# Performance work log

Hardware: AMD Instinct MI355X
Metric: run time of the kernel (lower is better)

The kernel has to match this reference:

```python
import jax, jax.numpy as jnp
import numpy as np

N = 50000
E = 800000
D = 512
H = 256
K = 16
COLLAPSE_REG = 1.0


def setup_inputs() -> dict:
    key = jax.random.key(0)
    ks = jax.random.split(key, 8)
    embeddings = jax.random.normal(ks[0], (N, D), dtype=jnp.float32)
    edge_src = jax.random.randint(ks[1], (E,), 0, N, dtype=jnp.int32)
    edge_dst = jax.random.randint(ks[2], (E,), 0, N, dtype=jnp.int32)
    # GCNConv params (glorot-ish scaling)
    W1 = jax.random.normal(ks[3], (D, H), dtype=jnp.float32) / np.sqrt(D)
    b1 = jnp.zeros((H,), dtype=jnp.float32)
    W2 = jax.random.normal(ks[4], (H, H), dtype=jnp.float32) / np.sqrt(H)
    b2 = jnp.zeros((H,), dtype=jnp.float32)
    Wa = jax.random.normal(ks[5], (H, K), dtype=jnp.float32) / np.sqrt(H)
    ba = jnp.zeros((K,), dtype=jnp.float32)
    return {"embeddings": embeddings, "edge_src": edge_src, "edge_dst": edge_dst,
            "W1": W1, "b1": b1, "W2": W2, "b2": b2, "Wa": Wa, "ba": ba}


def _gcn_conv(x, W, b, src, dst, dis):
    # PyG GCNConv: transform then D^{-1/2}(A+I)D^{-1/2} aggregation + bias.
    x = x @ W                                   # [N, out]
    norm = dis[src] * dis[dst]                  # [E]
    agg = jax.ops.segment_sum(x[src] * norm[:, None], dst, num_segments=N)
    agg = agg + (dis * dis)[:, None] * x        # self-loop term
    return agg + b


def reference(embeddings, edge_src, edge_dst, W1, b1, W2, b2, Wa, ba):
    # symmetric-norm degrees with self-loops (edge weight 1)
    deg = 1.0 + jax.ops.segment_sum(jnp.ones((E,), jnp.float32), edge_dst, num_segments=N)
    dis = jax.lax.rsqrt(deg)                    # deg > 0 always (self-loop)

    x = jax.nn.selu(_gcn_conv(embeddings, W1, b1, edge_src, edge_dst, dis))
    x_skip = x  # dropout is identity in eval
    x = jax.nn.selu(_gcn_conv(x, W2, b2, edge_src, edge_dst, dis))
    x = x + x_skip
    assignments = jax.nn.softmax(x @ Wa + ba, axis=1)   # [N, K]

    # ---- DMoN losses (faithful to original, incl. scalar normalizer) ----
    degrees = jax.ops.segment_sum(jnp.ones((E,), jnp.float32), edge_src, num_segments=N)  # row sums of A
    m = degrees.sum() / 2.0
    AS = jax.ops.segment_sum(assignments[edge_dst], edge_src, num_segments=N)  # A @ S, [N, K]
    trace_pooled = jnp.sum(assignments * AS)    # trace(S^T A S)
    dS = degrees @ assignments                  # [K]
    normalizer = jnp.dot(dS, dS) / (2.0 * m)    # scalar (as in original code)
    spectral_loss = -(trace_pooled - K * normalizer) / (2.0 * m)

    cluster_sizes = assignments.sum(axis=0)     # [K]
    collapse_loss = jnp.linalg.norm(cluster_sizes) / N * jnp.sqrt(jnp.float32(K)) - 1.0
    entropy = -jnp.sum(assignments * jnp.log(assignments + 1e-8)) / N
    entropy_loss = -0.1 * entropy
    total_loss = spectral_loss + COLLAPSE_REG * collapse_loss + entropy_loss

    pooled = (assignments / (cluster_sizes + 1e-8)).T @ embeddings  # [K, D]
    return (assignments, pooled, spectral_loss, COLLAPSE_REG * collapse_loss, total_loss, entropy_loss)
```

## Files before the change

kernel.cpp:

```cpp
#include <hip/hip_runtime.h>
#include <hip/hip_fp16.h>
#include <math.h>

#define NN 50000
#define EE 800000
#define DD 512
#define HH 256
#define KK 16
#define NB_SCAN 196

typedef _Float16 half8_t __attribute__((ext_vector_type(8)));
typedef float f32x4 __attribute__((ext_vector_type(4)));

__global__ void zero_kernel(int* __restrict__ p, int n) {
    int i = blockIdx.x * blockDim.x + threadIdx.x;
    if (i < n) p[i] = 0;
}

__global__ void count_kernel(const int4* __restrict__ src4, const int4* __restrict__ dst4,
                             int* __restrict__ indeg, int* __restrict__ outdeg) {
    int e = blockIdx.x * blockDim.x + threadIdx.x;
    if (e < EE / 4) {
        int4 s = src4[e], d = dst4[e];
        atomicAdd(&outdeg[s.x], 1); atomicAdd(&outdeg[s.y], 1);
        atomicAdd(&outdeg[s.z], 1); atomicAdd(&outdeg[s.w], 1);
        atomicAdd(&indeg[d.x], 1);  atomicAdd(&indeg[d.y], 1);
        atomicAdd(&indeg[d.z], 1);  atomicAdd(&indeg[d.w], 1);
    }
}

__global__ void scan_p1(const int* __restrict__ in, int* __restrict__ part, int n,
                        const int* __restrict__ outdeg, float* __restrict__ dis,
                        float* __restrict__ degf) {
    __shared__ int tile[256];
    int t = threadIdx.x;
    int i = blockIdx.x * 256 + t;
    int v = (i < n) ? in[i] : 0;
    tile[t] = v;
    if (i < n) {
        dis[i]  = 1.0f / sqrtf(1.0f + (float)v);
        degf[i] = (float)outdeg[i];
    }
    __syncthreads();
    for (int o = 128; o > 0; o >>= 1) {
        if (t < o) tile[t] += tile[t + o];
        __syncthreads();
    }
    if (t == 0) part[blockIdx.x] = tile[0];
}

__global__ void scan_p2(int* __restrict__ part, int nb, int* __restrict__ off_end) {
    __shared__ int tile[256];
    int t = threadIdx.x;
    int v = (t < nb) ? part[t] : 0;
    tile[t] = v;
    __syncthreads();
    for (int o = 1; o < 256; o <<= 1) {
        int x = (t >= o) ? tile[t - o] : 0;
        __syncthreads();
        tile[t] += x;
        __syncthreads();
    }
    if (t < nb) part[t] = tile[t] - v;
    if (t == 255) *off_end = tile[255];
}

__global__ void scan_p3(const int* __restrict__ in, const int* __restrict__ part,
                        int* __restrict__ out, int n) {
    __shared__ int tile[256];
    int t = threadIdx.x;
    int i = blockIdx.x * 256 + t;
    int v = (i < n) ? in[i] : 0;
    tile[t] = v;
    __syncthreads();
    for (int o = 1; o < 256; o <<= 1) {
        int x = (t >= o) ? tile[t - o] : 0;
        __syncthreads();
        tile[t] += x;
        __syncthreads();
    }
    if (i < n) out[i] = part[blockIdx.x] + tile[t] - v;
}

__global__ void scatter_kernel(const int4* __restrict__ src4, const int4* __restrict__ dst4,
                               const int* __restrict__ off, int* __restrict__ cur,
                               int* __restrict__ nbr) {
    int e = blockIdx.x * blockDim.x + threadIdx.x;
    if (e < EE / 4) {
        int4 s = src4[e], d = dst4[e];
        int p;
        p = atomicAdd(&cur[d.x], 1); nbr[off[d.x] + p] = s.x;
        p = atomicAdd(&cur[d.y], 1); nbr[off[d.y] + p] = s.y;
        p = atomicAdd(&cur[d.z], 1); nbr[off[d.z] + p] = s.z;
        p = atomicAdd(&cur[d.w], 1); nbr[off[d.w] + p] = s.w;
    }
}

__global__ void transpose_w(const float* __restrict__ W1, __half* __restrict__ Wt1,
                            const float* __restrict__ W2, __half* __restrict__ Wt2) {
    int i = blockIdx.x * 256 + threadIdx.x;
    if (i < DD * HH) {
        int k = i / HH, n = i % HH;
        Wt1[(size_t)n * DD + k] = __float2half(W1[i]);
    } else {
        int j = i - DD * HH;
        int k = j / HH, n = j % HH;
        Wt2[(size_t)n * HH + k] = __float2half(W2[j]);
    }
}

template <typename TA, int KDIM>
__global__ __launch_bounds__(256) void mfma_gemm(const TA* __restrict__ A,
                                                 const __half* __restrict__ Bt,
                                                 __half* __restrict__ C, int M) {
    constexpr bool F32 = sizeof(TA) == 4;
    constexpr int SROW = F32 ? 36 : 40;
    constexpr int EPG  = F32 ? 4 : 8;
    constexpr int GPR  = 32 / EPG;
    constexpr int RPP  = 256 / GPR;
    constexpr int NP   = 128 / RPP;
    constexpr int KI   = KDIM / 32;

    __shared__ TA As[2][128 * SROW];

    int t = threadIdx.x;
    int wave = t >> 6, lane = t & 63, quad = lane >> 4, l16 = lane & 15;
    int row0 = blockIdx.x * 128, col0 = blockIdx.y * 128;
    int wm = (wave & 1) * 64, wn = (wave >> 1) * 64;
    int srow = t / GPR, sg = t % GPR;

    f32x4 acc[4][4] = {};
    uint4 sreg[NP];
    uint4 bcur[4];

    const __half* brow[4];
#pragma unroll
    for (int ni = 0; ni < 4; ni++)
        brow[ni] = Bt + (size_t)(col0 + wn + ni * 16 + l16) * KDIM + quad * 8;

    auto gloadA = [&](int k0) {
#pragma unroll
        for (int p = 0; p < NP; p++) {
            int gr = row0 + p * RPP + srow;
            if (gr < M)
                sreg[p] = *(const uint4*)(A + (size_t)gr * KDIM + k0 + sg * EPG);
            else
                sreg[p] = make_uint4(0, 0, 0, 0);
        }
    };
    auto sstore = [&](int buf) {
#pragma unroll
        for (int p = 0; p < NP; p++)
            *(uint4*)&As[buf][(p * RPP + srow) * SROW + sg * EPG] = sreg[p];
    };

    gloadA(0);
#pragma unroll
    for (int ni = 0; ni < 4; ni++) bcur[ni] = *(const uint4*)(brow[ni]);
    sstore(0);
    __syncthreads();

#pragma unroll
    for (int i = 0; i < KI; i++) {
        int cur = i & 1;
        uint4 bnext[4];
        if (i + 1 < KI) {
            gloadA((i + 1) * 32);
#pragma unroll
            for (int ni = 0; ni < 4; ni++)
                bnext[ni] = *(const uint4*)(brow[ni] + (i + 1) * 32);
        }

        half8_t af[4];
#pragma unroll
        for (int mi = 0; mi < 4; mi++) {
            int row = wm + mi * 16 + l16;
            if constexpr (F32) {
                const float* pl = (const float*)&As[cur][0] + row * SROW + quad * 8;
                float4 x0 = *(const float4*)pl;
                float4 x1 = *(const float4*)(pl + 4);
                half8_t h;
                h[0] = (_Float16)x0.x; h[1] = (_Float16)x0.y;
                h[2] = (_Float16)x0.z; h[3] = (_Float16)x0.w;
                h[4] = (_Float16)x1.x; h[5] = (_Float16)x1.y;
                h[6] = (_Float16)x1.z; h[7] = (_Float16)x1.w;
                af[mi] = h;
            } else {
                af[mi] = *(const half8_t*)&As[cur][row * SROW + quad * 8];
            }
        }
#pragma unroll
        for (int mi = 0; mi < 4; mi++)
#pragma unroll
            for (int ni = 0; ni < 4; ni++)
                acc[mi][ni] = __builtin_amdgcn_mfma_f32_16x16x32_f16(
                    af[mi], *(half8_t*)&bcur[ni], acc[mi][ni], 0, 0, 0);

        if (i + 1 < KI) {
            sstore(cur ^ 1);
#pragma unroll
            for (int ni = 0; ni < 4; ni++) bcur[ni] = bnext[ni];
        }
        __syncthreads();
    }

#pragma unroll
    for (int mi = 0; mi < 4; mi++) {
#pragma unroll
        for (int r = 0; r < 4; r++) {
            int rr = row0 + wm + mi * 16 + quad * 4 + r;
            if (rr < M) {
#pragma unroll
                for (int ni = 0; ni < 4; ni++) {
                    C[(size_t)rr * HH + col0 + wn + ni * 16 + l16] =
                        __float2half(acc[mi][ni][r]);
                }
            }
        }
    }
}

__device__ inline void fma8(float* acc, uint4 raw, float w) {
    const __half2* h = (const __half2*)&raw;
#pragma unroll
    for (int i = 0; i < 4; i++) {
        float2 f = __half22float2(h[i]);
        acc[2 * i]     += w * f.x;
        acc[2 * i + 1] += w * f.y;
    }
}

__global__ __launch_bounds__(256) void agg_selu(const __half* __restrict__ T,
                                                const float* __restrict__ dis,
                                                const int* __restrict__ off,
                                                const int* __restrict__ nbr,
                                                const float* __restrict__ bias,
                                                const __half* skip, __half* out) {
    int t = threadIdx.x;
    int l32 = t & 31;
    int n = blockIdx.x * 8 + (t >> 5);
    int c = l32 * 8;
    float dn = dis[n];

    float acc[8];
#pragma unroll
    for (int i = 0; i < 8; i++) acc[i] = 0.f;
    fma8(acc, *(const uint4*)(T + (size_t)n * HH + c), dn * dn);

    int s0 = off[n], s1 = off[n + 1];
    for (int base = s0; base < s1; base += 32) {
        int cnt = min(32, s1 - base);
        int sidv = 0; float sdsv = 0.f;
        if (l32 < cnt) {
            sidv = nbr[base + l32];
            sdsv = dis[sidv] * dn;
        }
        int j = 0;
        for (; j + 4 <= cnt; j += 4) {
            int a0 = __shfl(sidv, j, 32),     a1 = __shfl(sidv, j + 1, 32);
            int a2 = __shfl(sidv, j + 2, 32), a3 = __shfl(sidv, j + 3, 32);
            float w0 = __shfl(sdsv, j, 32),     w1 = __shfl(sdsv, j + 1, 32);
            float w2 = __shfl(sdsv, j + 2, 32), w3 = __shfl(sdsv, j + 3, 32);
            uint4 r0 = *(const uint4*)(T + (size_t)a0 * HH + c);
            uint4 r1 = *(const uint4*)(T + (size_t)a1 * HH + c);
            uint4 r2 = *(const uint4*)(T + (size_t)a2 * HH + c);
            uint4 r3 = *(const uint4*)(T + (size_t)a3 * HH + c);
            fma8(acc, r0, w0); fma8(acc, r1, w1);
            fma8(acc, r2, w2); fma8(acc, r3, w3);
        }
        for (; j < cnt; j++) {
            int s = __shfl(sidv, j, 32);
            float w = __shfl(sdsv, j, 32);
            fma8(acc, *(const uint4*)(T + (size_t)s * HH + c), w);
        }
    }

    const float scale = 1.0507009873554805f;
    const float alpha = 1.6732632423543772f;
    float4 b0 = *(const float4*)(bias + c);
    float4 b1 = *(const float4*)(bias + c + 4);
    float bb[8] = {b0.x, b0.y, b0.z, b0.w, b1.x, b1.y, b1.z, b1.w};
    float sk8[8];
#pragma unroll
    for (int i = 0; i < 8; i++) sk8[i] = 0.f;
    if (skip) {
        uint4 raw = *(const uint4*)(skip + (size_t)n * HH + c);
        const __half2* h = (const __half2*)&raw;
#pragma unroll
        for (int i = 0; i < 4; i++) {
            float2 f = __half22float2(h[i]);
            sk8[2 * i] = f.x; sk8[2 * i + 1] = f.y;
        }
    }
    _Float16 res[8];
#pragma unroll
    for (int i = 0; i < 8; i++) {
        float v = acc[i] + bb[i];
        float r = v > 0.f ? scale * v : scale * alpha * expm1f(v);
        res[i] = (_Float16)(r + sk8[i]);
    }
    *(uint4*)(out + (size_t)n * HH + c) = *(uint4*)res;
}

__global__ __launch_bounds__(256) void assign_kernel(const __half* __restrict__ X,
                                                     const float* __restrict__ Wa,
                                                     const float* __restrict__ ba,
                                                     const float* __restrict__ degf,
                                                     float* __restrict__ out_assign,
                                                     __half* __restrict__ out_f16,
                                                     float* __restrict__ scal) {
    __shared__ float sWa[HH * KK];
    __shared__ float sX[16][HH];
    __shared__ float scs[KK], sdS[KK], sent_s;
    int t = threadIdx.x;
    int nb = blockIdx.x * 16;
    for (int i = t; i < HH * KK; i += 256) sWa[i] = Wa[i];
    for (int r = 0; r < 16; r++) sX[r][t] = __half2float(X[(size_t)(nb + r) * HH + t]);
    if (t < KK) { scs[t] = 0.f; sdS[t] = 0.f; }
    if (t == 0) sent_s = 0.f;
    __syncthreads();

    int k = t & 15, nl = t >> 4;
    float logit = ba[k];
    for (int c = 0; c < HH; c++) logit += sX[nl][c] * sWa[c * KK + k];

    float mx = logit;
    for (int o = 1; o < 16; o <<= 1) mx = fmaxf(mx, __shfl_xor(mx, o, 16));
    float e = expf(logit - mx);
    float sum = e;
    for (int o = 1; o < 16; o <<= 1) sum += __shfl_xor(sum, o, 16);
    float a = e / sum;
    int node = nb + nl;
    out_assign[(size_t)node * KK + k] = a;
    out_f16[(size_t)node * KK + k] = __float2half(a);

    atomicAdd(&scs[k], a);
    atomicAdd(&sdS[k], degf[node] * a);
    float ent = a * logf(a + 1e-8f);
    for (int o = 32; o >= 1; o >>= 1) ent += __shfl_xor(ent, o);
    if ((t & 63) == 0) atomicAdd(&sent_s, ent);
    __syncthreads();
    if (t < KK) {
        atomicAdd(&scal[t], scs[t]);
        atomicAdd(&scal[16 + t], sdS[t]);
    }
    if (t == 0) atomicAdd(&scal[33], sent_s);
}

__global__ __launch_bounds__(256) void edge_trace(const int* __restrict__ src,
                                                  const int* __restrict__ dst,
                                                  const __half* __restrict__ Ah,
                                                  float* __restrict__ scal) {
    int e = blockIdx.x * blockDim.x + threadIdx.x;
    float p = 0.f;
    if (e < EE) {
        int s = src[e], d = dst[e];
        uint4 sa = *(const uint4*)(Ah + (size_t)s * KK);
        uint4 sb = *(const uint4*)(Ah + (size_t)s * KK + 8);
        uint4 da = *(const uint4*)(Ah + (size_t)d * KK);
        uint4 db = *(const uint4*)(Ah + (size_t)d * KK + 8);
        const __half2* xs = (const __half2*)&sa;
        const __half2* xd = (const __half2*)&da;
#pragma unroll
        for (int i = 0; i < 4; i++) {
            float2 u = __half22float2(xs[i]), v = __half22float2(xd[i]);
            p += u.x * v.x + u.y * v.y;
        }
        xs = (const __half2*)&sb; xd = (const __half2*)&db;
#pragma unroll
        for (int i = 0; i < 4; i++) {
            float2 u = __half22float2(xs[i]), v = __half22float2(xd[i]);
            p += u.x * v.x + u.y * v.y;
        }
    }
    for (int o = 32; o >= 1; o >>= 1) p += __shfl_xor(p, o);
    __shared__ float sp;
    if (threadIdx.x == 0) sp = 0.f;
    __syncthreads();
    if ((threadIdx.x & 63) == 0) atomicAdd(&sp, p);
    __syncthreads();
    if (threadIdx.x == 0) atomicAdd(&scal[32], sp);
}

#define PCHUNK 250
__global__ __launch_bounds__(256) void pooled_partial(const float* __restrict__ emb,
                                                      const float* __restrict__ assign,
                                                      float* __restrict__ pool_acc) {
    int d = blockIdx.x * 256 + threadIdx.x;
    int c0 = blockIdx.y * PCHUNK;
    float acc[KK];
#pragma unroll
    for (int k = 0; k < KK; k++) acc[k] = 0.f;
    __shared__ float sa[128 * KK];
    for (int sub = 0; sub < PCHUNK; sub += 128) {
        int cnt = min(128, PCHUNK - sub);
        for (int i = threadIdx.x; i < cnt * KK; i += 256)
            sa[i] = assign[(size_t)(c0 + sub) * KK + i];
        __syncthreads();
        for (int j = 0; j < cnt; j++) {
            float ev = emb[(size_t)(c0 + sub + j) * DD + d];
#pragma unroll
            for (int k = 0; k < KK; k++) acc[k] += sa[j * KK + k] * ev;
        }
        __syncthreads();
    }
#pragma unroll
    for (int k = 0; k < KK; k++) atomicAdd(&pool_acc[k * DD + d], acc[k]);
}

__global__ void finalize(const float* __restrict__ pool_acc, const float* __restrict__ scal,
                         float* __restrict__ out) {
    int bx = blockIdx.x, t = threadIdx.x;
    if (bx < 32) {
        int i = bx * 256 + t;
        int k = i / DD;
        out[800000 + i] = pool_acc[i] / (scal[k] + 1e-8f);
    } else if (t == 0) {
        float cs2 = 0.f, ds2 = 0.f;
        for (int k = 0; k < KK; k++) {
            cs2 += scal[k] * scal[k];
            ds2 += scal[16 + k] * scal[16 + k];
        }
        float two_m = (float)EE;
        float normalizer = ds2 / two_m;
        float trace = scal[32];
        float spectral = -(trace - (float)KK * normalizer) / two_m;
        float collapse = sqrtf(cs2) / (float)NN * 4.0f - 1.0f;
        float entl = 0.1f * scal[33] / (float)NN;
        out[808192] = spectral;
        out[808193] = collapse;
        out[808194] = spectral + collapse + entl;
        out[808195] = entl;
    }
}

extern "C" void kernel_launch(void* const* d_in, const int* in_sizes, int n_in,
                              void* d_out, int out_size, void* d_ws, size_t ws_size,
                              hipStream_t stream) {
    const float* emb = (const float*)d_in[0];
    const int* esrc  = (const int*)d_in[1];
    const int* edst  = (const int*)d_in[2];
    const float* W1  = (const float*)d_in[3];
    const float* b1  = (const float*)d_in[4];
    const float* W2  = (const float*)d_in[5];
    const float* b2  = (const float*)d_in[6];
    const float* Wa  = (const float*)d_in[7];
    const float* ba  = (const float*)d_in[8];
    float* out = (float*)d_out;

    int* indeg      = (int*)d_ws;
    int* outdeg     = indeg + 50000;
    int* cur        = outdeg + 50000;
    float* pool_acc = (float*)(cur + 50000);
    float* scal     = pool_acc + 8192;
    int* part       = (int*)(scal + 64);
    int* off        = part + 256;
    int* nbr        = off + 50004;
    float* dis      = (float*)(nbr + 800000);
    float* degf     = dis + 50000;
    __half* Wt1     = (__half*)(degf + 50000);
    __half* Wt2     = Wt1 + 256 * 512;
    __half* T       = Wt2 + 256 * 256;
    __half* Hb      = T + (size_t)NN * HH;
    __half* Ah      = T;

    zero_kernel<<<dim3(619), 256, 0, stream>>>((int*)d_ws, 158256);
    count_kernel<<<dim3(782), 256, 0, stream>>>((const int4*)esrc, (const int4*)edst,
                                                indeg, outdeg);

    scan_p1<<<dim3(NB_SCAN), 256, 0, stream>>>(indeg, part, NN, outdeg, dis, degf);
    scan_p2<<<dim3(1), 256, 0, stream>>>(part, NB_SCAN, off + NN);
    scan_p3<<<dim3(NB_SCAN), 256, 0, stream>>>(indeg, part, off, NN);
    scatter_kernel<<<dim3(782), 256, 0, stream>>>((const int4*)esrc, (const int4*)edst,
                                                  off, cur, nbr);

    transpose_w<<<dim3(768), 256, 0, stream>>>(W1, Wt1, W2, Wt2);

    mfma_gemm<float, DD><<<dim3(392, 2), 256, 0, stream>>>(emb, Wt1, T, NN);
    agg_selu<<<dim3(6250), 256, 0, stream>>>(T, dis, off, nbr, b1, nullptr, Hb);

    mfma_gemm<__half, HH><<<dim3(392, 2), 256, 0, stream>>>(Hb, Wt2, T, NN);
    agg_selu<<<dim3(6250), 256, 0, stream>>>(T, dis, off, nbr, b2, Hb, Hb);

    assign_kernel<<<dim3(3125), 256, 0, stream>>>(Hb, Wa, ba, degf, out, Ah, scal);
    edge_trace<<<dim3(3125), 256, 0, stream>>>(esrc, edst, Ah, scal);
    pooled_partial<<<dim3(2, 200), 256, 0, stream>>>(emb, out, pool_acc);
    finalize<<<dim3(33), 256, 0, stream>>>(pool_acc, scal, out);
}
```

Before: 642.3 us.

## Use MFMA for assignment logits, vectorize edge trace, unroll aggregation, split pooling

The assignment logits are now computed with 16x16x32 f16 MFMA against a transposed half-precision Wa. Softmax and loss reductions run in registers with per-wave atomics, replacing the shared-memory scalar dot-product kernel. The edge-trace kernel reads int4 edge indices and processes four edges per thread. The aggregation loop unrolls to 8 neighbors for more loads in flight, and pooled_partial uses smaller chunks with float4 shared reads and twice as many blocks. The changes trade f16 precision in the logits and more global atomics for less instruction and launch overhead.

```diff
diff --git a/kernel.cpp b/kernel.cpp
--- a/kernel.cpp
+++ b/kernel.cpp
@@ -97,15 +97,20 @@
 }
 
 __global__ void transpose_w(const float* __restrict__ W1, __half* __restrict__ Wt1,
-                            const float* __restrict__ W2, __half* __restrict__ Wt2) {
+                            const float* __restrict__ W2, __half* __restrict__ Wt2,
+                            const float* __restrict__ Wa, __half* __restrict__ WaT) {
     int i = blockIdx.x * 256 + threadIdx.x;
     if (i < DD * HH) {
         int k = i / HH, n = i % HH;
         Wt1[(size_t)n * DD + k] = __float2half(W1[i]);
-    } else {
+    } else if (i < DD * HH + HH * HH) {
         int j = i - DD * HH;
         int k = j / HH, n = j % HH;
         Wt2[(size_t)n * HH + k] = __float2half(W2[j]);
+    } else if (i < DD * HH + HH * HH + HH * KK) {
+        int j = i - DD * HH - HH * HH;
+        int k = j / KK, n = j % KK;
+        WaT[n * HH + k] = __float2half(Wa[j]);
     }
 }
 
@@ -256,17 +261,27 @@
             sdsv = dis[sidv] * dn;
         }
         int j = 0;
-        for (; j + 4 <= cnt; j += 4) {
+        for (; j + 8 <= cnt; j += 8) {
             int a0 = __shfl(sidv, j, 32),     a1 = __shfl(sidv, j + 1, 32);
             int a2 = __shfl(sidv, j + 2, 32), a3 = __shfl(sidv, j + 3, 32);
+            int a4 = __shfl(sidv, j + 4, 32), a5 = __shfl(sidv, j + 5, 32);
+            int a6 = __shfl(sidv, j + 6, 32), a7 = __shfl(sidv, j + 7, 32);
             float w0 = __shfl(sdsv, j, 32),     w1 = __shfl(sdsv, j + 1, 32);
             float w2 = __shfl(sdsv, j + 2, 32), w3 = __shfl(sdsv, j + 3, 32);
+            float w4 = __shfl(sdsv, j + 4, 32), w5 = __shfl(sdsv, j + 5, 32);
+            float w6 = __shfl(sdsv, j + 6, 32), w7 = __shfl(sdsv, j + 7, 32);
             uint4 r0 = *(const uint4*)(T + (size_t)a0 * HH + c);
             uint4 r1 = *(const uint4*)(T + (size_t)a1 * HH + c);
             uint4 r2 = *(const uint4*)(T + (size_t)a2 * HH + c);
             uint4 r3 = *(const uint4*)(T + (size_t)a3 * HH + c);
+            uint4 r4 = *(const uint4*)(T + (size_t)a4 * HH + c);
+            uint4 r5 = *(const uint4*)(T + (size_t)a5 * HH + c);
+            uint4 r6 = *(const uint4*)(T + (size_t)a6 * HH + c);
+            uint4 r7 = *(const uint4*)(T + (size_t)a7 * HH + c);
             fma8(acc, r0, w0); fma8(acc, r1, w1);
             fma8(acc, r2, w2); fma8(acc, r3, w3);
+            fma8(acc, r4, w4); fma8(acc, r5, w5);
+            fma8(acc, r6, w6); fma8(acc, r7, w7);
         }
         for (; j < cnt; j++) {
             int s = __shfl(sidv, j, 32);
@@ -302,76 +317,102 @@
     *(uint4*)(out + (size_t)n * HH + c) = *(uint4*)res;
 }
 
-__global__ __launch_bounds__(256) void assign_kernel(const __half* __restrict__ X,
-                                                     const float* __restrict__ Wa,
-                                                     const float* __restrict__ ba,
-                                                     const float* __restrict__ degf,
-                                                     float* __restrict__ out_assign,
-                                                     __half* __restrict__ out_f16,
-                                                     float* __restrict__ scal) {
-    __shared__ float sWa[HH * KK];
-    __shared__ float sX[16][HH];
-    __shared__ float scs[KK], sdS[KK], sent_s;
+__global__ __launch_bounds__(256) void assign_mfma(const __half* __restrict__ Hb,
+                                                   const __half* __restrict__ WaT,
+                                                   const float* __restrict__ ba,
+                                                   const float* __restrict__ degf,
+                                                   float* __restrict__ out_assign,
+                                                   __half* __restrict__ out_f16,
+                                                   float* __restrict__ scal) {
     int t = threadIdx.x;
-    int nb = blockIdx.x * 16;
-    for (int i = t; i < HH * KK; i += 256) sWa[i] = Wa[i];
-    for (int r = 0; r < 16; r++) sX[r][t] = __half2float(X[(size_t)(nb + r) * HH + t]);
-    if (t < KK) { scs[t] = 0.f; sdS[t] = 0.f; }
-    if (t == 0) sent_s = 0.f;
-    __syncthreads();
-
-    int k = t & 15, nl = t >> 4;
-    float logit = ba[k];
-    for (int c = 0; c < HH; c++) logit += sX[nl][c] * sWa[c * KK + k];
-
-    float mx = logit;
-    for (int o = 1; o < 16; o <<= 1) mx = fmaxf(mx, __shfl_xor(mx, o, 16));
-    float e = expf(logit - mx);
-    float sum = e;
-    for (int o = 1; o < 16; o <<= 1) sum += __shfl_xor(sum, o, 16);
-    float a = e / sum;
-    int node = nb + nl;
-    out_assign[(size_t)node * KK + k] = a;
-    out_f16[(size_t)node * KK + k] = __float2half(a);
-
-    atomicAdd(&scs[k], a);
-    atomicAdd(&sdS[k], degf[node] * a);
-    float ent = a * logf(a + 1e-8f);
-    for (int o = 32; o >= 1; o >>= 1) ent += __shfl_xor(ent, o);
-    if ((t & 63) == 0) atomicAdd(&sent_s, ent);
-    __syncthreads();
-    if (t < KK) {
-        atomicAdd(&scal[t], scs[t]);
-        atomicAdd(&scal[16 + t], sdS[t]);
-    }
-    if (t == 0) atomicAdd(&scal[33], sent_s);
-}
-
-__global__ __launch_bounds__(256) void edge_trace(const int* __restrict__ src,
-                                                  const int* __restrict__ dst,
+    int wave = t >> 6, lane = t & 63, quad = lane >> 4, l16 = lane & 15;
+    int nb = blockIdx.x * 256 + wave * 64;
+
+    f32x4 acc[4] = {};
+    const __half* bp = WaT + l16 * HH + quad * 8;
+    const __half* ap[4];
+#pragma unroll
+    for (int mi = 0; mi < 4; mi++) {
+        int r = nb + mi * 16 + l16;
+        if (r >= NN) r = NN - 1;
+        ap[mi] = Hb + (size_t)r * HH + quad * 8;
+    }
+#pragma unroll
+    for (int s = 0; s < 8; s++) {
+        half8_t bf = *(const half8_t*)(bp + s * 32);
+#pragma unroll
+        for (int mi = 0; mi < 4; mi++) {
+            half8_t af = *(const half8_t*)(ap[mi] + s * 32);
+            acc[mi] = __builtin_amdgcn_mfma_f32_16x16x32_f16(af, bf, acc[mi], 0, 0, 0);
+        }
+    }
+
+    float myb = ba[l16];
+    float lcs = 0.f, ldS = 0.f, lent = 0.f;
+#pragma unroll
+    for (int mi = 0; mi < 4; mi++) {
+#pragma unroll
+        for (int r = 0; r < 4; r++) {
+            int node = nb + mi * 16 + quad * 4 + r;
+            bool ok = node < NN;
+            float logit = acc[mi][r] + myb;
+            float mx = logit;
+            for (int o = 1; o < 16; o <<= 1) mx = fmaxf(mx, __shfl_xor(mx, o, 16));
+            float e = expf(logit - mx);
+            float sum = e;
+            for (int o = 1; o < 16; o <<= 1) sum += __shfl_xor(sum, o, 16);
+            float a = e / sum;
+            if (ok) {
+                out_assign[(size_t)node * KK + l16] = a;
+                out_f16[(size_t)node * KK + l16] = __float2half(a);
+                lcs += a;
+                ldS += degf[node] * a;
+                lent += a * logf(a + 1e-8f);
+            }
+        }
+    }
+    lcs += __shfl_xor(lcs, 16); lcs += __shfl_xor(lcs, 32);
+    ldS += __shfl_xor(ldS, 16); ldS += __shfl_xor(ldS, 32);
+    for (int o = 32; o >= 1; o >>= 1) lent += __shfl_xor(lent, o);
+    if (quad == 0) {
+        atomicAdd(&scal[l16], lcs);
+        atomicAdd(&scal[16 + l16], ldS);
+    }
+    if (lane == 0) atomicAdd(&scal[33], lent);
+}
+
+__device__ inline float dot16h(const __half* a, const __half* b) {
+    uint4 a0 = *(const uint4*)a, a1 = *(const uint4*)(a + 8);
+    uint4 b0 = *(const uint4*)b, b1 = *(const uint4*)(b + 8);
+    float p = 0.f;
+    const __half2* xa = (const __half2*)&a0;
+    const __half2* xb = (const __half2*)&b0;
+#pragma unroll
+    for (int i = 0; i < 4; i++) {
+        float2 u = __half22float2(xa[i]), v = __half22float2(xb[i]);
+        p += u.x * v.x + u.y * v.y;
+    }
+    xa = (const __half2*)&a1; xb = (const __half2*)&b1;
+#pragma unroll
+    for (int i = 0; i < 4; i++) {
+        float2 u = __half22float2(xa[i]), v = __half22float2(xb[i]);
+        p += u.x * v.x + u.y * v.y;
+    }
+    return p;
+}
+
+__global__ __launch_bounds__(256) void edge_trace(const int4* __restrict__ src4,
+                                                  const int4* __restrict__ dst4,
                                                   const __half* __restrict__ Ah,
                                                   float* __restrict__ scal) {
     int e = blockIdx.x * blockDim.x + threadIdx.x;
     float p = 0.f;
-    if (e < EE) {
-        int s = src[e], d = dst[e];
-        uint4 sa = *(const uint4*)(Ah + (size_t)s * KK);
-        uint4 sb = *(const uint4*)(Ah + (size_t)s * KK + 8);
-        uint4 da = *(const uint4*)(Ah + (size_t)d * KK);
-        uint4 db = *(const uint4*)(Ah + (size_t)d * KK + 8);
-        const __half2* xs = (const __half2*)&sa;
-        const __half2* xd = (const __half2*)&da;
-#pragma unroll
-        for (int i = 0; i < 4; i++) {
-            float2 u = __half22float2(xs[i]), v = __half22float2(xd[i]);
-            p += u.x * v.x + u.y * v.y;
-        }
-        xs = (const __half2*)&sb; xd = (const __half2*)&db;
-#pragma unroll
-        for (int i = 0; i < 4; i++) {
-            float2 u = __half22float2(xs[i]), v = __half22float2(xd[i]);
-            p += u.x * v.x + u.y * v.y;
-        }
+    if (e < EE / 4) {
+        int4 s = src4[e], d = dst4[e];
+        p += dot16h(Ah + (size_t)s.x * KK, Ah + (size_t)d.x * KK);
+        p += dot16h(Ah + (size_t)s.y * KK, Ah + (size_t)d.y * KK);
+        p += dot16h(Ah + (size_t)s.z * KK, Ah + (size_t)d.z * KK);
+        p += dot16h(Ah + (size_t)s.w * KK, Ah + (size_t)d.w * KK);
     }
     for (int o = 32; o >= 1; o >>= 1) p += __shfl_xor(p, o);
     __shared__ float sp;
@@ -382,27 +423,32 @@
     if (threadIdx.x == 0) atomicAdd(&scal[32], sp);
 }
 
-#define PCHUNK 250
+#define PCH 125
 __global__ __launch_bounds__(256) void pooled_partial(const float* __restrict__ emb,
                                                       const float* __restrict__ assign,
                                                       float* __restrict__ pool_acc) {
     int d = blockIdx.x * 256 + threadIdx.x;
-    int c0 = blockIdx.y * PCHUNK;
+    int c0 = blockIdx.y * PCH;
     float acc[KK];
 #pragma unroll
     for (int k = 0; k < KK; k++) acc[k] = 0.f;
-    __shared__ float sa[128 * KK];
-    for (int sub = 0; sub < PCHUNK; sub += 128) {
-        int cnt = min(128, PCHUNK - sub);
-        for (int i = threadIdx.x; i < cnt * KK; i += 256)
-            sa[i] = assign[(size_t)(c0 + sub) * KK + i];
-        __syncthreads();
-        for (int j = 0; j < cnt; j++) {
-            float ev = emb[(size_t)(c0 + sub + j) * DD + d];
-#pragma unroll
-            for (int k = 0; k < KK; k++) acc[k] += sa[j * KK + k] * ev;
-        }
-        __syncthreads();
+    __shared__ float sa[PCH * KK];
+    {
+        const float4* srcv = (const float4*)(assign + (size_t)c0 * KK);
+        float4* dstv = (float4*)sa;
+        for (int i = threadIdx.x; i < PCH * KK / 4; i += 256) dstv[i] = srcv[i];
+    }
+    __syncthreads();
+    for (int j = 0; j < PCH; j++) {
+        float ev = emb[(size_t)(c0 + j) * DD + d];
+#pragma unroll
+        for (int k4 = 0; k4 < 4; k4++) {
+            float4 s4 = *(const float4*)&sa[j * KK + k4 * 4];
+            acc[k4 * 4 + 0] += s4.x * ev;
+            acc[k4 * 4 + 1] += s4.y * ev;
+            acc[k4 * 4 + 2] += s4.z * ev;
+            acc[k4 * 4 + 3] += s4.w * ev;
+        }
     }
 #pragma unroll
     for (int k = 0; k < KK; k++) atomicAdd(&pool_acc[k * DD + d], acc[k]);
@@ -460,7 +506,8 @@
     float* degf     = dis + 50000;
     __half* Wt1     = (__half*)(degf + 50000);
     __half* Wt2     = Wt1 + 256 * 512;
-    __half* T       = Wt2 + 256 * 256;
+    __half* WaT     = Wt2 + 256 * 256;
+    __half* T       = WaT + 16 * 256;
     __half* Hb      = T + (size_t)NN * HH;
     __half* Ah      = T;
 
@@ -474,7 +521,7 @@
     scatter_kernel<<<dim3(782), 256, 0, stream>>>((const int4*)esrc, (const int4*)edst,
                                                   off, cur, nbr);
 
-    transpose_w<<<dim3(768), 256, 0, stream>>>(W1, Wt1, W2, Wt2);
+    transpose_w<<<dim3(784), 256, 0, stream>>>(W1, Wt1, W2, Wt2, Wa, WaT);
 
     mfma_gemm<float, DD><<<dim3(392, 2), 256, 0, stream>>>(emb, Wt1, T, NN);
     agg_selu<<<dim3(6250), 256, 0, stream>>>(T, dis, off, nbr, b1, nullptr, Hb);
@@ -482,8 +529,8 @@
     mfma_gemm<__half, HH><<<dim3(392, 2), 256, 0, stream>>>(Hb, Wt2, T, NN);
     agg_selu<<<dim3(6250), 256, 0, stream>>>(T, dis, off, nbr, b2, Hb, Hb);
 
-    assign_kernel<<<dim3(3125), 256, 0, stream>>>(Hb, Wa, ba, degf, out, Ah, scal);
-    edge_trace<<<dim3(3125), 256, 0, stream>>>(esrc, edst, Ah, scal);
-    pooled_partial<<<dim3(2, 200), 256, 0, stream>>>(emb, out, pool_acc);
+    assign_mfma<<<dim3(196), 256, 0, stream>>>(Hb, WaT, ba, degf, out, Ah, scal);
+    edge_trace<<<dim3(782), 256, 0, stream>>>((const int4*)esrc, (const int4*)edst, Ah, scal);
+    pooled_partial<<<dim3(2, 400), 256, 0, stream>>>(emb, out, pool_acc);
     finalize<<<dim3(33), 256, 0, stream>>>(pool_acc, scal, out);
 }
```

New measurement: 563.8 us. 1.14x faster.
